# Kernel optimization log

Hardware: AMD Instinct MI355X
Metric: run time of the kernel (lower is better)

## Reference

```python
import jax, jax.numpy as jnp
import numpy as np

B, C, H, W = 8, 1, 384, 384
P, D, NH, L, E, HF = 16, 768, 12, 12, 4, 3072
Hp, Wp = H // P, W // P
N = Hp * Wp            # 576 tokens
DH = D // NH           # 64 per head
EPS = 1e-5


def setup_inputs() -> dict:
    key = jax.random.key(0)
    ks = jax.random.split(key, 10)
    g = lambda k, shp: (0.02 * jax.random.normal(k, shp, dtype=jnp.float32))
    return {
        "x": jax.random.normal(ks[0], (B, C, H, W), dtype=jnp.float32),
        "patch_w": g(ks[1], (D, C * P * P)),        # Conv2d(k=16,s=16) == unfold+matmul
        "patch_b": jnp.zeros((D,), jnp.float32),
        "pos_embed": g(ks[2], (1, N, D)),
        "ln1_g": jnp.ones((L, D), jnp.float32),
        "ln1_b": jnp.zeros((L, D), jnp.float32),
        "qkv_w": g(ks[3], (L, 3 * D, D)),           # torch MHA in_proj_weight
        "qkv_b": jnp.zeros((L, 3 * D), jnp.float32),
        "out_w": g(ks[4], (L, D, D)),
        "out_b": jnp.zeros((L, D), jnp.float32),
        "ln2_g": jnp.ones((L, D), jnp.float32),
        "ln2_b": jnp.zeros((L, D), jnp.float32),
        "gate_w": g(ks[5], (L, E, D)),
        "gate_b": jnp.zeros((L, E), jnp.float32),
        "w1": g(ks[6], (L, E, HF, D)),
        "b1": jnp.zeros((L, E, HF), jnp.float32),
        "w2": g(ks[7], (L, E, D, HF)),
        "b2": jnp.zeros((L, E, D), jnp.float32),
    }


def _ln(x, g, b):
    m = jnp.mean(x, -1, keepdims=True)
    v = jnp.var(x, -1, keepdims=True)
    return (x - m) * jax.lax.rsqrt(v + EPS) * g + b


def _layer(t, prm):
    (l1g, l1b, qw, qb, ow, ob, l2g, l2b, gw, gb, W1, B1, W2, B2) = prm
    # --- MHA (pre-LN, residual) ---
    h = _ln(t, l1g, l1b)
    qkv = h @ qw.T + qb                                   # [B,N,3D]
    q, k, v = jnp.split(qkv, 3, axis=-1)
    q = q.reshape(B, N, NH, DH).transpose(0, 2, 1, 3)     # [B,NH,N,DH]
    k = k.reshape(B, N, NH, DH).transpose(0, 2, 1, 3)
    v = v.reshape(B, N, NH, DH).transpose(0, 2, 1, 3)
    att = jax.nn.softmax(jnp.einsum('bhnd,bhmd->bhnm', q, k) / jnp.sqrt(jnp.float32(DH)), axis=-1)
    a = jnp.einsum('bhnm,bhmd->bhnd', att, v).transpose(0, 2, 1, 3).reshape(B, N, D)
    t = t + a @ ow.T + ob
    # --- MoE FFN, top_k=1: raw gate logits used as combine weights ---
    h2 = _ln(t, l2g, l2b)
    scores = h2 @ gw.T + gb                               # [B,N,E]
    idx = jnp.argmax(scores, axis=-1)                     # [B,N] chosen expert
    wgt = jnp.max(scores, axis=-1)                        # [B,N] raw logit weight
    hid = jax.nn.gelu(jnp.einsum('bnd,ehd->benh', h2, W1) + B1[None, :, None, :], approximate=False)
    y = jnp.einsum('benh,edh->bend', hid, W2) + B2[None, :, None, :]   # [B,E,N,D]
    sel = jax.nn.one_hot(idx, E, dtype=t.dtype) * wgt[..., None]       # [B,N,E]
    t = t + jnp.einsum('bend,bne->bnd', y, sel)
    return t, None


def reference(x, patch_w, patch_b, pos_embed, ln1_g, ln1_b, qkv_w, qkv_b,
              out_w, out_b, ln2_g, ln2_b, gate_w, gate_b, w1, b1, w2, b2):
    # patch embed: Conv2d(kernel=stride=P) == non-overlapping unfold + matmul
    patches = x.reshape(B, C, Hp, P, Wp, P).transpose(0, 2, 4, 1, 3, 5).reshape(B, N, C * P * P)
    tok = patches @ patch_w.T + patch_b + pos_embed
    layer = jax.checkpoint(_layer)
    tok, _ = jax.lax.scan(layer, tok,
                          (ln1_g, ln1_b, qkv_w, qkv_b, out_w, out_b,
                           ln2_g, ln2_b, gate_w, gate_b, w1, b1, w2, b2))
    # rearrange 'b (h w) c -> b c h w'
    return tok.reshape(B, Hp, Wp, D).transpose(0, 3, 1, 2)
```

## Files before the change

kernel.cpp:

```cpp
#include <hip/hip_runtime.h>
#include <cmath>

#define TOK 4608
#define DMODEL 768

typedef __attribute__((ext_vector_type(8))) _Float16 f16x8;
typedef __attribute__((ext_vector_type(4))) float f32x4;

__device__ __forceinline__ float gelu_exact(float x) {
    return 0.5f * x * (1.0f + erff(x * 0.70710678118654752440f));
}

__device__ __forceinline__ void cvt2(float x, unsigned short& h, unsigned short& m)
{
    _Float16 hf = (_Float16)x;
    float r = (x - (float)hf) * 2048.0f;
    _Float16 mf = (_Float16)r;
    h = __builtin_bit_cast(unsigned short, hf);
    m = __builtin_bit_cast(unsigned short, mf);
}

__device__ __forceinline__ void cvt2_pack8(const float4 a, const float4 b,
                                           uint4& H, uint4& M)
{
    unsigned short h[8], m[8];
    cvt2(a.x, h[0], m[0]); cvt2(a.y, h[1], m[1]);
    cvt2(a.z, h[2], m[2]); cvt2(a.w, h[3], m[3]);
    cvt2(b.x, h[4], m[4]); cvt2(b.y, h[5], m[5]);
    cvt2(b.z, h[6], m[6]); cvt2(b.w, h[7], m[7]);
    H = (uint4){ (unsigned)h[0] | ((unsigned)h[1] << 16), (unsigned)h[2] | ((unsigned)h[3] << 16),
                 (unsigned)h[4] | ((unsigned)h[5] << 16), (unsigned)h[6] | ((unsigned)h[7] << 16) };
    M = (uint4){ (unsigned)m[0] | ((unsigned)m[1] << 16), (unsigned)m[2] | ((unsigned)m[3] << 16),
                 (unsigned)m[4] | ((unsigned)m[5] << 16), (unsigned)m[6] | ((unsigned)m[7] << 16) };
}

__global__ __launch_bounds__(256)
void im2col_kernel(const float* __restrict__ x, float* __restrict__ patches)
{
    int idx = blockIdx.x*256 + threadIdx.x;
    int k = idx & 255, tokid = idx >> 8;
    int b = tokid / 576, n = tokid % 576;
    int hp = n / 24, wp = n % 24;
    patches[idx] = x[(size_t)b*147456 + (size_t)(hp*16 + (k >> 4))*384 + wp*16 + (k & 15)];
}

__global__ __launch_bounds__(256)
void ln_kernel(const float* __restrict__ in, float* __restrict__ out,
               const float* __restrict__ g, const float* __restrict__ bta)
{
    int tokid = blockIdx.x;
    const float* xr = in + (size_t)tokid*768;
    int t = threadIdx.x;
    float v0 = xr[t], v1 = xr[t+256], v2 = xr[t+512];
    float s = v0+v1+v2, q = v0*v0+v1*v1+v2*v2;
    for (int off = 32; off > 0; off >>= 1) {
        s += __shfl_down(s, off);
        q += __shfl_down(q, off);
    }
    __shared__ float ss[4], sq[4];
    int wv = t >> 6, ln = t & 63;
    if (ln == 0) { ss[wv] = s; sq[wv] = q; }
    __syncthreads();
    float ts = ss[0]+ss[1]+ss[2]+ss[3];
    float tq = sq[0]+sq[1]+sq[2]+sq[3];
    float mean = ts * (1.f/768.f);
    float var  = tq * (1.f/768.f) - mean*mean;
    float inv  = rsqrtf(var + 1e-5f);
    float* orow = out + (size_t)tokid*768;
    orow[t]     = (v0-mean)*inv*g[t]     + bta[t];
    orow[t+256] = (v1-mean)*inv*g[t+256] + bta[t+256];
    orow[t+512] = (v2-mean)*inv*g[t+512] + bta[t+512];
}

__global__ __launch_bounds__(256, 2)
void gemm_mfma(const float* __restrict__ A, const float* __restrict__ Bw,
               const float* __restrict__ bias, float* __restrict__ C,
               int M, int Nout, int K, int ldA, int ldC, int mode,
               const int* __restrict__ lists, const int* __restrict__ counts,
               const float* __restrict__ wgt)
{
    int Meff = M;
    const int* gather = nullptr;
    if (counts) {
        int e = blockIdx.z;
        Meff   = counts[e];
        gather = lists + e * TOK;
        Bw    += (size_t)e * Nout * K;
        bias  += (size_t)e * Nout;
    }
    int m0 = blockIdx.y << 7, n0 = blockIdx.x << 7;
    if (m0 >= Meff) return;

    __shared__ unsigned short Ah[128][40];
    __shared__ unsigned short Am[128][40];
    __shared__ unsigned short Bh[128][40];
    __shared__ unsigned short Bm[128][40];

    int t = threadIdx.x;
    int srow = t >> 1;
    int koff = (t & 1) << 4;

    int ar = m0 + srow;
    long agrow = -1;
    if (ar < Meff) agrow = gather ? gather[ar] : ar;
    const float* Asrc = (agrow >= 0) ? (A + (size_t)agrow*ldA + koff) : nullptr;
    const float* Bsrc = Bw + (size_t)(n0 + srow)*K + koff;

    int lane = t & 63;
    int wv   = t >> 6;
    int wm   = (wv >> 1) << 6;
    int wn   = (wv & 1) << 6;
    int r16  = lane & 15;
    int g    = lane >> 4;

    f32x4 acc1[4][4], acc2[4][4];
    #pragma unroll
    for (int i = 0; i < 4; ++i)
        #pragma unroll
        for (int j = 0; j < 4; ++j) {
            acc1[i][j] = (f32x4){0.f, 0.f, 0.f, 0.f};
            acc2[i][j] = (f32x4){0.f, 0.f, 0.f, 0.f};
        }

    float4 ra[4], rb[4];
    ra[0] = ra[1] = ra[2] = ra[3] = make_float4(0.f, 0.f, 0.f, 0.f);

    auto load_tile = [&](int k0) {
        if (Asrc) {
            ra[0] = *(const float4*)(Asrc + k0);
            ra[1] = *(const float4*)(Asrc + k0 + 4);
            ra[2] = *(const float4*)(Asrc + k0 + 8);
            ra[3] = *(const float4*)(Asrc + k0 + 12);
        }
        rb[0] = *(const float4*)(Bsrc + k0);
        rb[1] = *(const float4*)(Bsrc + k0 + 4);
        rb[2] = *(const float4*)(Bsrc + k0 + 8);
        rb[3] = *(const float4*)(Bsrc + k0 + 12);
    };

    auto stage = [&]() {
        uint4 H, M_;
        cvt2_pack8(ra[0], ra[1], H, M_);
        *(uint4*)&Ah[srow][koff]     = H;
        *(uint4*)&Am[srow][koff]     = M_;
        cvt2_pack8(ra[2], ra[3], H, M_);
        *(uint4*)&Ah[srow][koff + 8] = H;
        *(uint4*)&Am[srow][koff + 8] = M_;
        cvt2_pack8(rb[0], rb[1], H, M_);
        *(uint4*)&Bh[srow][koff]     = H;
        *(uint4*)&Bm[srow][koff]     = M_;
        cvt2_pack8(rb[2], rb[3], H, M_);
        *(uint4*)&Bh[srow][koff + 8] = H;
        *(uint4*)&Bm[srow][koff + 8] = M_;
    };

    load_tile(0);

    for (int k0 = 0; k0 < K; k0 += 32) {
        __syncthreads();
        stage();
        __syncthreads();
        if (k0 + 32 < K) load_tile(k0 + 32);

        f16x8 fah[4], fam[4];
        #pragma unroll
        for (int i = 0; i < 4; ++i) {
            int ml = wm + i*16 + r16;
            fah[i] = *(const f16x8*)&Ah[ml][g*8];
            fam[i] = *(const f16x8*)&Am[ml][g*8];
        }
        #pragma unroll
        for (int j = 0; j < 4; ++j) {
            int nl = wn + j*16 + r16;
            f16x8 fbh = *(const f16x8*)&Bh[nl][g*8];
            f16x8 fbm = *(const f16x8*)&Bm[nl][g*8];
            #pragma unroll
            for (int i = 0; i < 4; ++i) {
                acc1[i][j] = __builtin_amdgcn_mfma_f32_16x16x32_f16(fah[i], fbh, acc1[i][j], 0, 0, 0);
                acc2[i][j] = __builtin_amdgcn_mfma_f32_16x16x32_f16(fah[i], fbm, acc2[i][j], 0, 0, 0);
                acc2[i][j] = __builtin_amdgcn_mfma_f32_16x16x32_f16(fam[i], fbh, acc2[i][j], 0, 0, 0);
            }
        }
    }

    const float MS = 1.0f / 2048.0f;
    float biasv[4];
    #pragma unroll
    for (int j = 0; j < 4; ++j) biasv[j] = bias[n0 + wn + j*16 + r16];

    #pragma unroll
    for (int i = 0; i < 4; ++i) {
        int mb = m0 + wm + i*16 + (g << 2);
        #pragma unroll
        for (int r = 0; r < 4; ++r) {
            int m = mb + r;
            if (m >= Meff) continue;
            int row = gather ? gather[m] : m;
            float* crow = C + (size_t)row*ldC + n0 + wn + r16;
            float w = (mode == 3) ? wgt[row] : 0.f;
            #pragma unroll
            for (int j = 0; j < 4; ++j) {
                float val = acc1[i][j][r] + acc2[i][j][r] * MS + biasv[j];
                float* cp = crow + j*16;
                if      (mode == 0) *cp = val;
                else if (mode == 1) *cp += val;
                else if (mode == 2) *cp = gelu_exact(val);
                else if (mode == 3) *cp += w * val;
                else {
                    *cp = val + wgt[(size_t)(row % 576)*768 + n0 + wn + j*16 + r16];
                }
            }
        }
    }
}

__global__ __launch_bounds__(256)
void attn_kernel(const float* __restrict__ qkv, float* __restrict__ attn)
{
    int q0 = blockIdx.x << 6;
    int h  = blockIdx.y;
    int b  = blockIdx.z;
    const float* base = qkv + (size_t)b * 576 * 2304;
    int qoff = h << 6, koff = 768 + (h << 6), voff = 1536 + (h << 6);

    __shared__ unsigned short Qh[64][72], Qm[64][72];
    __shared__ unsigned short Kh[64][72], Km[64][72];
    __shared__ unsigned short Vth[64][72], Vtm[64][72];
    __shared__ unsigned short Ph[64][72], Pm[64][72];

    int t    = threadIdx.x;
    int lane = t & 63;
    int wq   = t >> 6;
    int l15  = lane & 15;
    int g    = lane >> 4;

    int srow = t >> 2;
    int sq   = t & 3;

    {
        const float* src = &base[(size_t)(q0 + srow)*2304 + qoff + (sq << 4)];
        #pragma unroll
        for (int k = 0; k < 16; k += 4) {
            float4 v = *(const float4*)(src + k);
            ushort4 hh, mm;
            cvt2(v.x, hh.x, mm.x); cvt2(v.y, hh.y, mm.y);
            cvt2(v.z, hh.z, mm.z); cvt2(v.w, hh.w, mm.w);
            *(ushort4*)&Qh[srow][(sq << 4) + k] = hh;
            *(ushort4*)&Qm[srow][(sq << 4) + k] = mm;
        }
    }
    __syncthreads();

    f16x8 fqh[2], fqm[2];
    #pragma unroll
    for (int ks = 0; ks < 2; ++ks) {
        fqh[ks] = *(const f16x8*)&Qh[wq*16 + l15][ks*32 + g*8];
        fqm[ks] = *(const f16x8*)&Qm[wq*16 + l15][ks*32 + g*8];
    }

    float4 rk[4], rv[4];
    {
        const float* ks_ = &base[(size_t)srow*2304 + koff + (sq << 4)];
        const float* vs_ = &base[(size_t)srow*2304 + voff + (sq << 2)];
        #pragma unroll
        for (int k = 0; k < 4; ++k) rk[k] = *(const float4*)(ks_ + 4*k);
        #pragma unroll
        for (int k = 0; k < 4; ++k) rv[k] = *(const float4*)(vs_ + 16*k);
    }

    f32x4 o1[4], o2[4];
    #pragma unroll
    for (int df = 0; df < 4; ++df) {
        o1[df] = (f32x4){0.f,0.f,0.f,0.f};
        o2[df] = (f32x4){0.f,0.f,0.f,0.f};
    }
    float m_[4] = {-3.4e38f,-3.4e38f,-3.4e38f,-3.4e38f};
    float l_[4] = {0.f,0.f,0.f,0.f};
    const float MS = 1.0f / 2048.0f;

    for (int j0 = 0; j0 < 576; j0 += 64) {
        __syncthreads();
        #pragma unroll
        for (int k = 0; k < 4; ++k) {
            ushort4 hh, mm;
            cvt2(rk[k].x, hh.x, mm.x); cvt2(rk[k].y, hh.y, mm.y);
            cvt2(rk[k].z, hh.z, mm.z); cvt2(rk[k].w, hh.w, mm.w);
            *(ushort4*)&Kh[srow][(sq << 4) + 4*k] = hh;
            *(ushort4*)&Km[srow][(sq << 4) + 4*k] = mm;
        }
        #pragma unroll
        for (int k = 0; k < 4; ++k) {
            ushort4 hh, mm;
            cvt2(rv[k].x, hh.x, mm.x); cvt2(rv[k].y, hh.y, mm.y);
            cvt2(rv[k].z, hh.z, mm.z); cvt2(rv[k].w, hh.w, mm.w);
            int dbase = (sq << 2) + (k << 4);
            Vth[dbase+0][srow] = hh.x; Vtm[dbase+0][srow] = mm.x;
            Vth[dbase+1][srow] = hh.y; Vtm[dbase+1][srow] = mm.y;
            Vth[dbase+2][srow] = hh.z; Vtm[dbase+2][srow] = mm.z;
            Vth[dbase+3][srow] = hh.w; Vtm[dbase+3][srow] = mm.w;
        }
        __syncthreads();
        int jn = j0 + 64;
        if (jn < 576) {
            const float* ks_ = &base[(size_t)(jn + srow)*2304 + koff + (sq << 4)];
            const float* vs_ = &base[(size_t)(jn + srow)*2304 + voff + (sq << 2)];
            #pragma unroll
            for (int k = 0; k < 4; ++k) rk[k] = *(const float4*)(ks_ + 4*k);
            #pragma unroll
            for (int k = 0; k < 4; ++k) rv[k] = *(const float4*)(vs_ + 16*k);
        }

        f32x4 s1[4], s2[4];
        #pragma unroll
        for (int jf = 0; jf < 4; ++jf) {
            s1[jf] = (f32x4){0.f,0.f,0.f,0.f};
            s2[jf] = (f32x4){0.f,0.f,0.f,0.f};
        }
        #pragma unroll
        for (int jf = 0; jf < 4; ++jf) {
            #pragma unroll
            for (int ks = 0; ks < 2; ++ks) {
                f16x8 fkh = *(const f16x8*)&Kh[jf*16 + l15][ks*32 + g*8];
                f16x8 fkm = *(const f16x8*)&Km[jf*16 + l15][ks*32 + g*8];
                s1[jf] = __builtin_amdgcn_mfma_f32_16x16x32_f16(fqh[ks], fkh, s1[jf], 0, 0, 0);
                s2[jf] = __builtin_amdgcn_mfma_f32_16x16x32_f16(fqh[ks], fkm, s2[jf], 0, 0, 0);
                s2[jf] = __builtin_amdgcn_mfma_f32_16x16x32_f16(fqm[ks], fkh, s2[jf], 0, 0, 0);
            }
        }
        float p[4][4];
        #pragma unroll
        for (int jf = 0; jf < 4; ++jf)
            #pragma unroll
            for (int r = 0; r < 4; ++r)
                p[jf][r] = (s1[jf][r] + s2[jf][r]*MS) * 0.125f;

        #pragma unroll
        for (int r = 0; r < 4; ++r) {
            float tm = fmaxf(fmaxf(p[0][r], p[1][r]), fmaxf(p[2][r], p[3][r]));
            #pragma unroll
            for (int off = 8; off > 0; off >>= 1) tm = fmaxf(tm, __shfl_xor(tm, off, 16));
            float mn = fmaxf(m_[r], tm);
            float f  = expf(m_[r] - mn);
            m_[r] = mn;
            l_[r] *= f;
            #pragma unroll
            for (int df = 0; df < 4; ++df) { o1[df][r] *= f; o2[df][r] *= f; }
            float ps = 0.f;
            #pragma unroll
            for (int jf = 0; jf < 4; ++jf) {
                p[jf][r] = expf(p[jf][r] - mn);
                ps += p[jf][r];
            }
            #pragma unroll
            for (int off = 8; off > 0; off >>= 1) ps += __shfl_xor(ps, off, 16);
            l_[r] += ps;
        }
        #pragma unroll
        for (int jf = 0; jf < 4; ++jf)
            #pragma unroll
            for (int r = 0; r < 4; ++r) {
                unsigned short ph, pm;
                cvt2(p[jf][r], ph, pm);
                Ph[wq*16 + g*4 + r][jf*16 + l15] = ph;
                Pm[wq*16 + g*4 + r][jf*16 + l15] = pm;
            }

        #pragma unroll
        for (int ks = 0; ks < 2; ++ks) {
            f16x8 fph = *(const f16x8*)&Ph[wq*16 + l15][ks*32 + g*8];
            f16x8 fpm = *(const f16x8*)&Pm[wq*16 + l15][ks*32 + g*8];
            #pragma unroll
            for (int df = 0; df < 4; ++df) {
                f16x8 fvh = *(const f16x8*)&Vth[df*16 + l15][ks*32 + g*8];
                f16x8 fvm = *(const f16x8*)&Vtm[df*16 + l15][ks*32 + g*8];
                o1[df] = __builtin_amdgcn_mfma_f32_16x16x32_f16(fph, fvh, o1[df], 0, 0, 0);
                o2[df] = __builtin_amdgcn_mfma_f32_16x16x32_f16(fph, fvm, o2[df], 0, 0, 0);
                o2[df] = __builtin_amdgcn_mfma_f32_16x16x32_f16(fpm, fvh, o2[df], 0, 0, 0);
            }
        }
    }

    #pragma unroll
    for (int r = 0; r < 4; ++r) {
        float inv = 1.f / l_[r];
        size_t row = (size_t)(b*576 + q0 + wq*16 + g*4 + r)*768 + qoff + l15;
        #pragma unroll
        for (int df = 0; df < 4; ++df)
            attn[row + df*16] = (o1[df][r] + o2[df][r]*MS) * inv;
    }
}

__global__ __launch_bounds__(256)
void gate_kernel(const float* __restrict__ h2, const float* __restrict__ gw,
                 const float* __restrict__ gb, float* __restrict__ wgt,
                 int* __restrict__ lists, int* __restrict__ counts)
{
    int tokid = blockIdx.x;
    int t = threadIdx.x;
    const float* hr = h2 + (size_t)tokid*768;
    float p0=0.f,p1=0.f,p2=0.f,p3=0.f;
    for (int k = t; k < 768; k += 256) {
        float hv = hr[k];
        p0 = fmaf(hv, gw[k],        p0);
        p1 = fmaf(hv, gw[768 + k],  p1);
        p2 = fmaf(hv, gw[1536 + k], p2);
        p3 = fmaf(hv, gw[2304 + k], p3);
    }
    for (int off = 32; off > 0; off >>= 1) {
        p0 += __shfl_down(p0, off);
        p1 += __shfl_down(p1, off);
        p2 += __shfl_down(p2, off);
        p3 += __shfl_down(p3, off);
    }
    __shared__ float red[4][4];
    int wv = t >> 6, ln = t & 63;
    if (ln == 0) { red[wv][0]=p0; red[wv][1]=p1; red[wv][2]=p2; red[wv][3]=p3; }
    __syncthreads();
    if (t == 0) {
        float s[4];
        #pragma unroll
        for (int e = 0; e < 4; ++e)
            s[e] = red[0][e]+red[1][e]+red[2][e]+red[3][e] + gb[e];
        int best = 0; float bv = s[0];
        #pragma unroll
        for (int e = 1; e < 4; ++e) if (s[e] > bv) { bv = s[e]; best = e; }
        wgt[tokid] = bv;
        int pos = atomicAdd(&counts[best], 1);
        lists[best*TOK + pos] = tokid;
    }
}

__global__ void zero_counts(int* counts) { if (threadIdx.x < 4) counts[threadIdx.x] = 0; }

__global__ __launch_bounds__(256)
void out_transpose(const float* __restrict__ tok, float* __restrict__ out)
{
    int idx = blockIdx.x*256 + threadIdx.x;
    int wp = idx % 24;
    int hp = (idx / 24) % 24;
    int d  = (idx / 576) % 768;
    int b  = idx / (576*768);
    out[idx] = tok[(size_t)(b*576 + hp*24 + wp)*768 + d];
}

extern "C" void kernel_launch(void* const* d_in, const int* in_sizes, int n_in,
                              void* d_out, int out_size, void* d_ws, size_t ws_size,
                              hipStream_t stream)
{
    const float* x       = (const float*)d_in[0];
    const float* patch_w = (const float*)d_in[1];
    const float* patch_b = (const float*)d_in[2];
    const float* pos     = (const float*)d_in[3];
    const float* ln1_g   = (const float*)d_in[4];
    const float* ln1_b   = (const float*)d_in[5];
    const float* qkv_w   = (const float*)d_in[6];
    const float* qkv_b   = (const float*)d_in[7];
    const float* out_w   = (const float*)d_in[8];
    const float* out_b   = (const float*)d_in[9];
    const float* ln2_g   = (const float*)d_in[10];
    const float* ln2_b   = (const float*)d_in[11];
    const float* gate_w  = (const float*)d_in[12];
    const float* gate_b  = (const float*)d_in[13];
    const float* w1      = (const float*)d_in[14];
    const float* b1      = (const float*)d_in[15];
    const float* w2      = (const float*)d_in[16];
    const float* b2      = (const float*)d_in[17];
    float* out = (float*)d_out;

    float* ws    = (float*)d_ws;
    float* tok   = ws;
    float* h     = ws + 3538944;
    float* scr   = ws + 7077888;
    float* qkv   = scr;
    float* attn  = scr + 10616832;
    float* hid   = scr;
    float* patches = scr;
    float* wgt   = ws + 21233664;
    int*   lists = (int*)(ws + 21238272);
    int*   counts= (int*)(ws + 21256704);

    im2col_kernel<<<4608, 256, 0, stream>>>(x, patches);
    gemm_mfma<<<dim3(6,36,1), 256, 0, stream>>>(patches, patch_w, patch_b, tok,
                                                4608, 768, 256, 256, 768, 4,
                                                nullptr, nullptr, pos);

    for (int l = 0; l < 12; ++l) {
        ln_kernel<<<4608, 256, 0, stream>>>(tok, h, ln1_g + l*768, ln1_b + l*768);
        gemm_mfma<<<dim3(18,36,1), 256, 0, stream>>>(h, qkv_w + (size_t)l*2304*768, qkv_b + l*2304,
                                                     qkv, 4608, 2304, 768, 768, 2304, 0,
                                                     nullptr, nullptr, nullptr);
        attn_kernel<<<dim3(9,12,8), 256, 0, stream>>>(qkv, attn);
        gemm_mfma<<<dim3(6,36,1), 256, 0, stream>>>(attn, out_w + (size_t)l*768*768, out_b + l*768,
                                                    tok, 4608, 768, 768, 768, 768, 1,
                                                    nullptr, nullptr, nullptr);
        ln_kernel<<<4608, 256, 0, stream>>>(tok, h, ln2_g + l*768, ln2_b + l*768);
        zero_counts<<<1, 64, 0, stream>>>(counts);
        gate_kernel<<<4608, 256, 0, stream>>>(h, gate_w + l*3072, gate_b + l*4, wgt, lists, counts);
        gemm_mfma<<<dim3(24,36,4), 256, 0, stream>>>(h, w1 + (size_t)l*4*3072*768, b1 + (size_t)l*4*3072,
                                                     hid, 4608, 3072, 768, 768, 3072, 2,
                                                     lists, counts, nullptr);
        gemm_mfma<<<dim3(6,36,4), 256, 0, stream>>>(hid, w2 + (size_t)l*4*768*3072, b2 + (size_t)l*4*768,
                                                    tok, 4608, 768, 3072, 3072, 768, 3,
                                                    lists, counts, wgt);
    }
    out_transpose<<<13824, 256, 0, stream>>>(tok, out);
}
```

Before: 8.237 ms.

## Store activations and weights as pre-split fp16 hi/lo planes for GEMM and attention

Each producer kernel (LN, QKV GEMM, attention, W1 GEMM with GELU, im2col) now writes its output as two fp16 planes (high part and scaled residual) instead of fp32. Weights are converted into the same two-plane form once per layer by a new cvt_plane kernel. The GEMM and attention inner loops then copy these planes straight into shared memory with no per-tile conversion, and the activation traffic they read is about halved. In exchange there are extra conversion launches and a weight pass every layer (w1/w2 are large), plus more workspace.

```diff
diff --git a/kernel.cpp b/kernel.cpp
--- a/kernel.cpp
+++ b/kernel.cpp
@@ -6,6 +6,7 @@
 
 typedef __attribute__((ext_vector_type(8))) _Float16 f16x8;
 typedef __attribute__((ext_vector_type(4))) float f32x4;
+typedef unsigned short ushort_t;
 
 __device__ __forceinline__ float gelu_exact(float x) {
     return 0.5f * x * (1.0f + erff(x * 0.70710678118654752440f));
@@ -20,32 +21,41 @@
     m = __builtin_bit_cast(unsigned short, mf);
 }
 
-__device__ __forceinline__ void cvt2_pack8(const float4 a, const float4 b,
-                                           uint4& H, uint4& M)
-{
-    unsigned short h[8], m[8];
-    cvt2(a.x, h[0], m[0]); cvt2(a.y, h[1], m[1]);
-    cvt2(a.z, h[2], m[2]); cvt2(a.w, h[3], m[3]);
-    cvt2(b.x, h[4], m[4]); cvt2(b.y, h[5], m[5]);
-    cvt2(b.z, h[6], m[6]); cvt2(b.w, h[7], m[7]);
-    H = (uint4){ (unsigned)h[0] | ((unsigned)h[1] << 16), (unsigned)h[2] | ((unsigned)h[3] << 16),
-                 (unsigned)h[4] | ((unsigned)h[5] << 16), (unsigned)h[6] | ((unsigned)h[7] << 16) };
-    M = (uint4){ (unsigned)m[0] | ((unsigned)m[1] << 16), (unsigned)m[2] | ((unsigned)m[3] << 16),
-                 (unsigned)m[4] | ((unsigned)m[5] << 16), (unsigned)m[6] | ((unsigned)m[7] << 16) };
+__device__ __forceinline__ float tof(unsigned short u) {
+    return (float)__builtin_bit_cast(_Float16, u);
 }
 
 __global__ __launch_bounds__(256)
-void im2col_kernel(const float* __restrict__ x, float* __restrict__ patches)
+void cvt_plane(const float* __restrict__ src, ushort_t* __restrict__ dh,
+               ushort_t* __restrict__ dm, int n)
+{
+    int i = (blockIdx.x*256 + threadIdx.x) << 2;
+    if (i >= n) return;
+    float4 v = *(const float4*)(src + i);
+    ushort4 H, M;
+    cvt2(v.x, H.x, M.x); cvt2(v.y, H.y, M.y);
+    cvt2(v.z, H.z, M.z); cvt2(v.w, H.w, M.w);
+    *(ushort4*)(dh + i) = H;
+    *(ushort4*)(dm + i) = M;
+}
+
+__global__ __launch_bounds__(256)
+void im2col_kernel(const float* __restrict__ x, ushort_t* __restrict__ ph,
+                   ushort_t* __restrict__ pm)
 {
     int idx = blockIdx.x*256 + threadIdx.x;
     int k = idx & 255, tokid = idx >> 8;
     int b = tokid / 576, n = tokid % 576;
     int hp = n / 24, wp = n % 24;
-    patches[idx] = x[(size_t)b*147456 + (size_t)(hp*16 + (k >> 4))*384 + wp*16 + (k & 15)];
+    float v = x[(size_t)b*147456 + (size_t)(hp*16 + (k >> 4))*384 + wp*16 + (k & 15)];
+    unsigned short hh, mm;
+    cvt2(v, hh, mm);
+    ph[idx] = hh; pm[idx] = mm;
 }
 
 __global__ __launch_bounds__(256)
-void ln_kernel(const float* __restrict__ in, float* __restrict__ out,
+void ln_kernel(const float* __restrict__ in, ushort_t* __restrict__ outh,
+               ushort_t* __restrict__ outm,
                const float* __restrict__ g, const float* __restrict__ bta)
 {
     int tokid = blockIdx.x;
@@ -66,15 +76,21 @@
     float mean = ts * (1.f/768.f);
     float var  = tq * (1.f/768.f) - mean*mean;
     float inv  = rsqrtf(var + 1e-5f);
-    float* orow = out + (size_t)tokid*768;
-    orow[t]     = (v0-mean)*inv*g[t]     + bta[t];
-    orow[t+256] = (v1-mean)*inv*g[t+256] + bta[t+256];
-    orow[t+512] = (v2-mean)*inv*g[t+512] + bta[t+512];
+    size_t base = (size_t)tokid*768;
+    unsigned short hh, mm;
+    float y0 = (v0-mean)*inv*g[t]     + bta[t];
+    float y1 = (v1-mean)*inv*g[t+256] + bta[t+256];
+    float y2 = (v2-mean)*inv*g[t+512] + bta[t+512];
+    cvt2(y0, hh, mm); outh[base+t]     = hh; outm[base+t]     = mm;
+    cvt2(y1, hh, mm); outh[base+t+256] = hh; outm[base+t+256] = mm;
+    cvt2(y2, hh, mm); outh[base+t+512] = hh; outm[base+t+512] = mm;
 }
 
 __global__ __launch_bounds__(256, 2)
-void gemm_mfma(const float* __restrict__ A, const float* __restrict__ Bw,
+void gemm_mfma(const ushort_t* __restrict__ Ahp, const ushort_t* __restrict__ Amp,
+               const ushort_t* __restrict__ Bhp, const ushort_t* __restrict__ Bmp,
                const float* __restrict__ bias, float* __restrict__ C,
+               ushort_t* __restrict__ Chp, ushort_t* __restrict__ Cmp,
                int M, int Nout, int K, int ldA, int ldC, int mode,
                const int* __restrict__ lists, const int* __restrict__ counts,
                const float* __restrict__ wgt)
@@ -85,7 +101,8 @@
         int e = blockIdx.z;
         Meff   = counts[e];
         gather = lists + e * TOK;
-        Bw    += (size_t)e * Nout * K;
+        Bhp   += (size_t)e * Nout * K;
+        Bmp   += (size_t)e * Nout * K;
         bias  += (size_t)e * Nout;
     }
     int m0 = blockIdx.y << 7, n0 = blockIdx.x << 7;
@@ -103,8 +120,10 @@
     int ar = m0 + srow;
     long agrow = -1;
     if (ar < Meff) agrow = gather ? gather[ar] : ar;
-    const float* Asrc = (agrow >= 0) ? (A + (size_t)agrow*ldA + koff) : nullptr;
-    const float* Bsrc = Bw + (size_t)(n0 + srow)*K + koff;
+    const ushort_t* Ah_src = (agrow >= 0) ? (Ahp + (size_t)agrow*ldA + koff) : nullptr;
+    const ushort_t* Am_src = (agrow >= 0) ? (Amp + (size_t)agrow*ldA + koff) : nullptr;
+    const ushort_t* Bh_src = Bhp + (size_t)(n0 + srow)*K + koff;
+    const ushort_t* Bm_src = Bmp + (size_t)(n0 + srow)*K + koff;
 
     int lane = t & 63;
     int wv   = t >> 6;
@@ -122,43 +141,34 @@
             acc2[i][j] = (f32x4){0.f, 0.f, 0.f, 0.f};
         }
 
-    float4 ra[4], rb[4];
-    ra[0] = ra[1] = ra[2] = ra[3] = make_float4(0.f, 0.f, 0.f, 0.f);
+    uint4 rah[2], ram[2], rbh[2], rbm[2];
+    rah[0] = rah[1] = ram[0] = ram[1] = (uint4){0u,0u,0u,0u};
 
     auto load_tile = [&](int k0) {
-        if (Asrc) {
-            ra[0] = *(const float4*)(Asrc + k0);
-            ra[1] = *(const float4*)(Asrc + k0 + 4);
-            ra[2] = *(const float4*)(Asrc + k0 + 8);
-            ra[3] = *(const float4*)(Asrc + k0 + 12);
-        }
-        rb[0] = *(const float4*)(Bsrc + k0);
-        rb[1] = *(const float4*)(Bsrc + k0 + 4);
-        rb[2] = *(const float4*)(Bsrc + k0 + 8);
-        rb[3] = *(const float4*)(Bsrc + k0 + 12);
-    };
-
-    auto stage = [&]() {
-        uint4 H, M_;
-        cvt2_pack8(ra[0], ra[1], H, M_);
-        *(uint4*)&Ah[srow][koff]     = H;
-        *(uint4*)&Am[srow][koff]     = M_;
-        cvt2_pack8(ra[2], ra[3], H, M_);
-        *(uint4*)&Ah[srow][koff + 8] = H;
-        *(uint4*)&Am[srow][koff + 8] = M_;
-        cvt2_pack8(rb[0], rb[1], H, M_);
-        *(uint4*)&Bh[srow][koff]     = H;
-        *(uint4*)&Bm[srow][koff]     = M_;
-        cvt2_pack8(rb[2], rb[3], H, M_);
-        *(uint4*)&Bh[srow][koff + 8] = H;
-        *(uint4*)&Bm[srow][koff + 8] = M_;
+        if (Ah_src) {
+            rah[0] = *(const uint4*)(Ah_src + k0);
+            rah[1] = *(const uint4*)(Ah_src + k0 + 8);
+            ram[0] = *(const uint4*)(Am_src + k0);
+            ram[1] = *(const uint4*)(Am_src + k0 + 8);
+        }
+        rbh[0] = *(const uint4*)(Bh_src + k0);
+        rbh[1] = *(const uint4*)(Bh_src + k0 + 8);
+        rbm[0] = *(const uint4*)(Bm_src + k0);
+        rbm[1] = *(const uint4*)(Bm_src + k0 + 8);
     };
 
     load_tile(0);
 
     for (int k0 = 0; k0 < K; k0 += 32) {
         __syncthreads();
-        stage();
+        *(uint4*)&Ah[srow][koff]   = rah[0];
+        *(uint4*)&Ah[srow][koff+8] = rah[1];
+        *(uint4*)&Am[srow][koff]   = ram[0];
+        *(uint4*)&Am[srow][koff+8] = ram[1];
+        *(uint4*)&Bh[srow][koff]   = rbh[0];
+        *(uint4*)&Bh[srow][koff+8] = rbh[1];
+        *(uint4*)&Bm[srow][koff]   = rbm[0];
+        *(uint4*)&Bm[srow][koff+8] = rbm[1];
         __syncthreads();
         if (k0 + 32 < K) load_tile(k0 + 32);
 
@@ -196,18 +206,26 @@
             int m = mb + r;
             if (m >= Meff) continue;
             int row = gather ? gather[m] : m;
-            float* crow = C + (size_t)row*ldC + n0 + wn + r16;
+            size_t rowoff = (size_t)row*ldC + n0 + wn + r16;
             float w = (mode == 3) ? wgt[row] : 0.f;
             #pragma unroll
             for (int j = 0; j < 4; ++j) {
                 float val = acc1[i][j][r] + acc2[i][j][r] * MS + biasv[j];
-                float* cp = crow + j*16;
-                if      (mode == 0) *cp = val;
-                else if (mode == 1) *cp += val;
-                else if (mode == 2) *cp = gelu_exact(val);
-                else if (mode == 3) *cp += w * val;
-                else {
-                    *cp = val + wgt[(size_t)(row % 576)*768 + n0 + wn + j*16 + r16];
+                size_t off = rowoff + j*16;
+                if (mode == 0) {
+                    unsigned short hh, mm;
+                    cvt2(val, hh, mm);
+                    Chp[off] = hh; Cmp[off] = mm;
+                } else if (mode == 1) {
+                    C[off] += val;
+                } else if (mode == 2) {
+                    unsigned short hh, mm;
+                    cvt2(gelu_exact(val), hh, mm);
+                    Chp[off] = hh; Cmp[off] = mm;
+                } else if (mode == 3) {
+                    C[off] += w * val;
+                } else {
+                    C[off] = val + wgt[(size_t)(row % 576)*768 + n0 + wn + j*16 + r16];
                 }
             }
         }
@@ -215,13 +233,14 @@
 }
 
 __global__ __launch_bounds__(256)
-void attn_kernel(const float* __restrict__ qkv, float* __restrict__ attn)
+void attn_kernel(const ushort_t* __restrict__ qh, const ushort_t* __restrict__ qm,
+                 ushort_t* __restrict__ aoh, ushort_t* __restrict__ aom)
 {
     int q0 = blockIdx.x << 6;
     int h  = blockIdx.y;
     int b  = blockIdx.z;
-    const float* base = qkv + (size_t)b * 576 * 2304;
-    int qoff = h << 6, koff = 768 + (h << 6), voff = 1536 + (h << 6);
+    size_t bbase = (size_t)b * 576 * 2304;
+    int qoff = h << 6, koff2 = 768 + (h << 6), voff = 1536 + (h << 6);
 
     __shared__ unsigned short Qh[64][72], Qm[64][72];
     __shared__ unsigned short Kh[64][72], Km[64][72];
@@ -238,16 +257,12 @@
     int sq   = t & 3;
 
     {
-        const float* src = &base[(size_t)(q0 + srow)*2304 + qoff + (sq << 4)];
-        #pragma unroll
-        for (int k = 0; k < 16; k += 4) {
-            float4 v = *(const float4*)(src + k);
-            ushort4 hh, mm;
-            cvt2(v.x, hh.x, mm.x); cvt2(v.y, hh.y, mm.y);
-            cvt2(v.z, hh.z, mm.z); cvt2(v.w, hh.w, mm.w);
-            *(ushort4*)&Qh[srow][(sq << 4) + k] = hh;
-            *(ushort4*)&Qm[srow][(sq << 4) + k] = mm;
-        }
+        const ushort_t* sh = qh + bbase + (size_t)(q0 + srow)*2304 + qoff + (sq << 4);
+        const ushort_t* sm = qm + bbase + (size_t)(q0 + srow)*2304 + qoff + (sq << 4);
+        *(uint4*)&Qh[srow][(sq<<4)]   = *(const uint4*)(sh);
+        *(uint4*)&Qh[srow][(sq<<4)+8] = *(const uint4*)(sh + 8);
+        *(uint4*)&Qm[srow][(sq<<4)]   = *(const uint4*)(sm);
+        *(uint4*)&Qm[srow][(sq<<4)+8] = *(const uint4*)(sm + 8);
     }
     __syncthreads();
 
@@ -258,15 +273,22 @@
         fqm[ks] = *(const f16x8*)&Qm[wq*16 + l15][ks*32 + g*8];
     }
 
-    float4 rk[4], rv[4];
-    {
-        const float* ks_ = &base[(size_t)srow*2304 + koff + (sq << 4)];
-        const float* vs_ = &base[(size_t)srow*2304 + voff + (sq << 2)];
-        #pragma unroll
-        for (int k = 0; k < 4; ++k) rk[k] = *(const float4*)(ks_ + 4*k);
-        #pragma unroll
-        for (int k = 0; k < 4; ++k) rv[k] = *(const float4*)(vs_ + 16*k);
-    }
+    uint4 pkh[2], pkm[2];
+    uint2 pvh[4], pvm[4];
+    auto fetch_kv = [&](int j0) {
+        const ushort_t* kh_ = qh + bbase + (size_t)(j0 + srow)*2304 + koff2 + (sq << 4);
+        const ushort_t* km_ = qm + bbase + (size_t)(j0 + srow)*2304 + koff2 + (sq << 4);
+        pkh[0] = *(const uint4*)(kh_);     pkh[1] = *(const uint4*)(kh_ + 8);
+        pkm[0] = *(const uint4*)(km_);     pkm[1] = *(const uint4*)(km_ + 8);
+        const ushort_t* vh_ = qh + bbase + (size_t)(j0 + srow)*2304 + voff + (sq << 2);
+        const ushort_t* vm_ = qm + bbase + (size_t)(j0 + srow)*2304 + voff + (sq << 2);
+        #pragma unroll
+        for (int k = 0; k < 4; ++k) {
+            pvh[k] = *(const uint2*)(vh_ + (k << 4));
+            pvm[k] = *(const uint2*)(vm_ + (k << 4));
+        }
+    };
+    fetch_kv(0);
 
     f32x4 o1[4], o2[4];
     #pragma unroll
@@ -280,35 +302,23 @@
 
     for (int j0 = 0; j0 < 576; j0 += 64) {
         __syncthreads();
+        *(uint4*)&Kh[srow][(sq<<4)]   = pkh[0];
+        *(uint4*)&Kh[srow][(sq<<4)+8] = pkh[1];
+        *(uint4*)&Km[srow][(sq<<4)]   = pkm[0];
+        *(uint4*)&Km[srow][(sq<<4)+8] = pkm[1];
         #pragma unroll
         for (int k = 0; k < 4; ++k) {
-            ushort4 hh, mm;
-            cvt2(rk[k].x, hh.x, mm.x); cvt2(rk[k].y, hh.y, mm.y);
-            cvt2(rk[k].z, hh.z, mm.z); cvt2(rk[k].w, hh.w, mm.w);
-            *(ushort4*)&Kh[srow][(sq << 4) + 4*k] = hh;
-            *(ushort4*)&Km[srow][(sq << 4) + 4*k] = mm;
-        }
-        #pragma unroll
-        for (int k = 0; k < 4; ++k) {
-            ushort4 hh, mm;
-            cvt2(rv[k].x, hh.x, mm.x); cvt2(rv[k].y, hh.y, mm.y);
-            cvt2(rv[k].z, hh.z, mm.z); cvt2(rv[k].w, hh.w, mm.w);
+            const ushort_t* ph = (const ushort_t*)&pvh[k];
+            const ushort_t* pm = (const ushort_t*)&pvm[k];
             int dbase = (sq << 2) + (k << 4);
-            Vth[dbase+0][srow] = hh.x; Vtm[dbase+0][srow] = mm.x;
-            Vth[dbase+1][srow] = hh.y; Vtm[dbase+1][srow] = mm.y;
-            Vth[dbase+2][srow] = hh.z; Vtm[dbase+2][srow] = mm.z;
-            Vth[dbase+3][srow] = hh.w; Vtm[dbase+3][srow] = mm.w;
+            Vth[dbase+0][srow] = ph[0]; Vtm[dbase+0][srow] = pm[0];
+            Vth[dbase+1][srow] = ph[1]; Vtm[dbase+1][srow] = pm[1];
+            Vth[dbase+2][srow] = ph[2]; Vtm[dbase+2][srow] = pm[2];
+            Vth[dbase+3][srow] = ph[3]; Vtm[dbase+3][srow] = pm[3];
         }
         __syncthreads();
         int jn = j0 + 64;
-        if (jn < 576) {
-            const float* ks_ = &base[(size_t)(jn + srow)*2304 + koff + (sq << 4)];
-            const float* vs_ = &base[(size_t)(jn + srow)*2304 + voff + (sq << 2)];
-            #pragma unroll
-            for (int k = 0; k < 4; ++k) rk[k] = *(const float4*)(ks_ + 4*k);
-            #pragma unroll
-            for (int k = 0; k < 4; ++k) rv[k] = *(const float4*)(vs_ + 16*k);
-        }
+        if (jn < 576) fetch_kv(jn);
 
         f32x4 s1[4], s2[4];
         #pragma unroll
@@ -383,24 +393,31 @@
     #pragma unroll
     for (int r = 0; r < 4; ++r) {
         float inv = 1.f / l_[r];
-        size_t row = (size_t)(b*576 + q0 + wq*16 + g*4 + r)*768 + qoff + l15;
-        #pragma unroll
-        for (int df = 0; df < 4; ++df)
-            attn[row + df*16] = (o1[df][r] + o2[df][r]*MS) * inv;
+        size_t rowoff = (size_t)(b*576 + q0 + wq*16 + g*4 + r)*768 + qoff + l15;
+        #pragma unroll
+        for (int df = 0; df < 4; ++df) {
+            float ov = (o1[df][r] + o2[df][r]*MS) * inv;
+            unsigned short hh, mm;
+            cvt2(ov, hh, mm);
+            aoh[rowoff + df*16] = hh;
+            aom[rowoff + df*16] = mm;
+        }
     }
 }
 
 __global__ __launch_bounds__(256)
-void gate_kernel(const float* __restrict__ h2, const float* __restrict__ gw,
-                 const float* __restrict__ gb, float* __restrict__ wgt,
-                 int* __restrict__ lists, int* __restrict__ counts)
+void gate_kernel(const ushort_t* __restrict__ hh, const ushort_t* __restrict__ hm,
+                 const float* __restrict__ gw, const float* __restrict__ gb,
+                 float* __restrict__ wgt, int* __restrict__ lists, int* __restrict__ counts)
 {
     int tokid = blockIdx.x;
     int t = threadIdx.x;
-    const float* hr = h2 + (size_t)tokid*768;
+    const ushort_t* hrh = hh + (size_t)tokid*768;
+    const ushort_t* hrm = hm + (size_t)tokid*768;
+    const float MS = 1.0f / 2048.0f;
     float p0=0.f,p1=0.f,p2=0.f,p3=0.f;
     for (int k = t; k < 768; k += 256) {
-        float hv = hr[k];
+        float hv = tof(hrh[k]) + tof(hrm[k]) * MS;
         p0 = fmaf(hv, gw[k],        p0);
         p1 = fmaf(hv, gw[768 + k],  p1);
         p2 = fmaf(hv, gw[1536 + k], p2);
@@ -467,40 +484,62 @@
     const float* b2      = (const float*)d_in[17];
     float* out = (float*)d_out;
 
-    float* ws    = (float*)d_ws;
-    float* tok   = ws;
-    float* h     = ws + 3538944;
-    float* scr   = ws + 7077888;
-    float* qkv   = scr;
-    float* attn  = scr + 10616832;
-    float* hid   = scr;
-    float* patches = scr;
-    float* wgt   = ws + 21233664;
-    int*   lists = (int*)(ws + 21238272);
-    int*   counts= (int*)(ws + 21256704);
-
-    im2col_kernel<<<4608, 256, 0, stream>>>(x, patches);
-    gemm_mfma<<<dim3(6,36,1), 256, 0, stream>>>(patches, patch_w, patch_b, tok,
+    char* wsb = (char*)d_ws;
+    size_t OF = 0;
+    float*    tok   = (float*)(wsb + OF);    OF += 14155776;
+    ushort_t* h_h   = (ushort_t*)(wsb + OF); OF += 7077888;
+    ushort_t* h_m   = (ushort_t*)(wsb + OF); OF += 7077888;
+    ushort_t* qkvh  = (ushort_t*)(wsb + OF); OF += 21233664;
+    ushort_t* qkvm  = (ushort_t*)(wsb + OF); OF += 21233664;
+    ushort_t* at_h  = (ushort_t*)(wsb + OF); OF += 7077888;
+    ushort_t* at_m  = (ushort_t*)(wsb + OF); OF += 7077888;
+    ushort_t* hid_h = (ushort_t*)(wsb + OF); OF += 28311552;
+    ushort_t* hid_m = (ushort_t*)(wsb + OF); OF += 28311552;
+    ushort_t* w_h   = (ushort_t*)(wsb + OF); OF += 42467328;
+    ushort_t* w_m   = (ushort_t*)(wsb + OF); OF += 42467328;
+    float*    wgt   = (float*)(wsb + OF);    OF += 18432;
+    int*      lists = (int*)(wsb + OF);      OF += 73728;
+    int*      counts= (int*)(wsb + OF);      OF += 16;
+
+    const size_t SEG_QKV = 0;
+    const size_t SEG_OUT = 1769472;
+    const size_t SEG_W1  = SEG_OUT + 589824;
+    const size_t SEG_W2  = SEG_W1  + 9437184;
+
+    im2col_kernel<<<4608, 256, 0, stream>>>(x, hid_h, hid_m);
+    cvt_plane<<<192, 256, 0, stream>>>(patch_w, w_h, w_m, 196608);
+    gemm_mfma<<<dim3(6,36,1), 256, 0, stream>>>(hid_h, hid_m, w_h, w_m, patch_b,
+                                                tok, nullptr, nullptr,
                                                 4608, 768, 256, 256, 768, 4,
                                                 nullptr, nullptr, pos);
 
     for (int l = 0; l < 12; ++l) {
-        ln_kernel<<<4608, 256, 0, stream>>>(tok, h, ln1_g + l*768, ln1_b + l*768);
-        gemm_mfma<<<dim3(18,36,1), 256, 0, stream>>>(h, qkv_w + (size_t)l*2304*768, qkv_b + l*2304,
-                                                     qkv, 4608, 2304, 768, 768, 2304, 0,
+        cvt_plane<<<1728, 256, 0, stream>>>(qkv_w + (size_t)l*1769472, w_h + SEG_QKV, w_m + SEG_QKV, 1769472);
+        cvt_plane<<< 576, 256, 0, stream>>>(out_w + (size_t)l*589824,  w_h + SEG_OUT, w_m + SEG_OUT, 589824);
+        cvt_plane<<<9216, 256, 0, stream>>>(w1 + (size_t)l*9437184,    w_h + SEG_W1,  w_m + SEG_W1,  9437184);
+        cvt_plane<<<9216, 256, 0, stream>>>(w2 + (size_t)l*9437184,    w_h + SEG_W2,  w_m + SEG_W2,  9437184);
+
+        ln_kernel<<<4608, 256, 0, stream>>>(tok, h_h, h_m, ln1_g + l*768, ln1_b + l*768);
+        gemm_mfma<<<dim3(18,36,1), 256, 0, stream>>>(h_h, h_m, w_h + SEG_QKV, w_m + SEG_QKV,
+                                                     qkv_b + l*2304, nullptr, qkvh, qkvm,
+                                                     4608, 2304, 768, 768, 2304, 0,
                                                      nullptr, nullptr, nullptr);
-        attn_kernel<<<dim3(9,12,8), 256, 0, stream>>>(qkv, attn);
-        gemm_mfma<<<dim3(6,36,1), 256, 0, stream>>>(attn, out_w + (size_t)l*768*768, out_b + l*768,
-                                                    tok, 4608, 768, 768, 768, 768, 1,
+        attn_kernel<<<dim3(9,12,8), 256, 0, stream>>>(qkvh, qkvm, at_h, at_m);
+        gemm_mfma<<<dim3(6,36,1), 256, 0, stream>>>(at_h, at_m, w_h + SEG_OUT, w_m + SEG_OUT,
+                                                    out_b + l*768, tok, nullptr, nullptr,
+                                                    4608, 768, 768, 768, 768, 1,
                                                     nullptr, nullptr, nullptr);
-        ln_kernel<<<4608, 256, 0, stream>>>(tok, h, ln2_g + l*768, ln2_b + l*768);
+        ln_kernel<<<4608, 256, 0, stream>>>(tok, h_h, h_m, ln2_g + l*768, ln2_b + l*768);
         zero_counts<<<1, 64, 0, stream>>>(counts);
-        gate_kernel<<<4608, 256, 0, stream>>>(h, gate_w + l*3072, gate_b + l*4, wgt, lists, counts);
-        gemm_mfma<<<dim3(24,36,4), 256, 0, stream>>>(h, w1 + (size_t)l*4*3072*768, b1 + (size_t)l*4*3072,
-                                                     hid, 4608, 3072, 768, 768, 3072, 2,
+        gate_kernel<<<4608, 256, 0, stream>>>(h_h, h_m, gate_w + l*3072, gate_b + l*4,
+                                              wgt, lists, counts);
+        gemm_mfma<<<dim3(24,36,4), 256, 0, stream>>>(h_h, h_m, w_h + SEG_W1, w_m + SEG_W1,
+                                                     b1 + (size_t)l*4*3072, nullptr, hid_h, hid_m,
+                                                     4608, 3072, 768, 768, 3072, 2,
                                                      lists, counts, nullptr);
-        gemm_mfma<<<dim3(6,36,4), 256, 0, stream>>>(hid, w2 + (size_t)l*4*768*3072, b2 + (size_t)l*4*768,
-                                                    tok, 4608, 768, 3072, 3072, 768, 3,
+        gemm_mfma<<<dim3(6,36,4), 256, 0, stream>>>(hid_h, hid_m, w_h + SEG_W2, w_m + SEG_W2,
+                                                    b2 + (size_t)l*4*768, tok, nullptr, nullptr,
+                                                    4608, 768, 3072, 3072, 768, 3,
                                                     lists, counts, wgt);
     }
     out_transpose<<<13824, 256, 0, stream>>>(tok, out);
```

Result: slower. 11.87 ms (+44.1%).

## Split GEMM into 128-tile and 64-tile variants with workgroup swizzle

Applied to the files above, without the earlier changes.

Replaces the single 128x128 GEMM with two templated kernels. gemm_big keeps 128x128 tiles for the QKV and W1 projections. gemm_small uses 64x64 tiles with a 64-deep K step for the N=768 GEMMs (patch embed, out-proj, W2), which gives those launches more workgroups and better CU fill. An optional block-ID swizzle remaps workgroup order across 8 groups, likely targeting the MI355X's XCD dispatch so neighbouring tiles share cache. Occupancy hint is raised to 3. The small tiles trade more global reloads of A and B for the extra parallelism.

```diff
diff --git a/kernel.cpp b/kernel.cpp
--- a/kernel.cpp
+++ b/kernel.cpp
@@ -72,12 +72,13 @@
     orow[t+512] = (v2-mean)*inv*g[t+512] + bta[t+512];
 }
 
-__global__ __launch_bounds__(256, 2)
-void gemm_mfma(const float* __restrict__ A, const float* __restrict__ Bw,
-               const float* __restrict__ bias, float* __restrict__ C,
-               int M, int Nout, int K, int ldA, int ldC, int mode,
-               const int* __restrict__ lists, const int* __restrict__ counts,
-               const float* __restrict__ wgt)
+template<bool SWZ>
+__global__ __launch_bounds__(256, 3)
+void gemm_big(const float* __restrict__ A, const float* __restrict__ Bw,
+              const float* __restrict__ bias, float* __restrict__ C,
+              int M, int Nout, int K, int ldA, int ldC, int mode,
+              const int* __restrict__ lists, const int* __restrict__ counts,
+              const float* __restrict__ wgt)
 {
     int Meff = M;
     const int* gather = nullptr;
@@ -88,7 +89,13 @@
         Bw    += (size_t)e * Nout * K;
         bias  += (size_t)e * Nout;
     }
-    int m0 = blockIdx.y << 7, n0 = blockIdx.x << 7;
+    int gx  = gridDim.x;
+    int bid = blockIdx.y * gx + blockIdx.x;
+    if constexpr (SWZ) {
+        int nwg = gx * gridDim.y;
+        bid = (bid & 7) * (nwg >> 3) + (bid >> 3);
+    }
+    int m0 = (bid / gx) << 7, n0 = (bid % gx) << 7;
     if (m0 >= Meff) return;
 
     __shared__ unsigned short Ah[128][40];
@@ -138,27 +145,25 @@
         rb[3] = *(const float4*)(Bsrc + k0 + 12);
     };
 
-    auto stage = [&]() {
-        uint4 H, M_;
-        cvt2_pack8(ra[0], ra[1], H, M_);
-        *(uint4*)&Ah[srow][koff]     = H;
-        *(uint4*)&Am[srow][koff]     = M_;
-        cvt2_pack8(ra[2], ra[3], H, M_);
-        *(uint4*)&Ah[srow][koff + 8] = H;
-        *(uint4*)&Am[srow][koff + 8] = M_;
-        cvt2_pack8(rb[0], rb[1], H, M_);
-        *(uint4*)&Bh[srow][koff]     = H;
-        *(uint4*)&Bm[srow][koff]     = M_;
-        cvt2_pack8(rb[2], rb[3], H, M_);
-        *(uint4*)&Bh[srow][koff + 8] = H;
-        *(uint4*)&Bm[srow][koff + 8] = M_;
-    };
-
     load_tile(0);
 
     for (int k0 = 0; k0 < K; k0 += 32) {
         __syncthreads();
-        stage();
+        {
+            uint4 H, M_;
+            cvt2_pack8(ra[0], ra[1], H, M_);
+            *(uint4*)&Ah[srow][koff]   = H;
+            *(uint4*)&Am[srow][koff]   = M_;
+            cvt2_pack8(ra[2], ra[3], H, M_);
+            *(uint4*)&Ah[srow][koff+8] = H;
+            *(uint4*)&Am[srow][koff+8] = M_;
+            cvt2_pack8(rb[0], rb[1], H, M_);
+            *(uint4*)&Bh[srow][koff]   = H;
+            *(uint4*)&Bm[srow][koff]   = M_;
+            cvt2_pack8(rb[2], rb[3], H, M_);
+            *(uint4*)&Bh[srow][koff+8] = H;
+            *(uint4*)&Bm[srow][koff+8] = M_;
+        }
         __syncthreads();
         if (k0 + 32 < K) load_tile(k0 + 32);
 
@@ -196,19 +201,165 @@
             int m = mb + r;
             if (m >= Meff) continue;
             int row = gather ? gather[m] : m;
-            float* crow = C + (size_t)row*ldC + n0 + wn + r16;
+            size_t rowoff = (size_t)row*ldC + n0 + wn + r16;
             float w = (mode == 3) ? wgt[row] : 0.f;
             #pragma unroll
             for (int j = 0; j < 4; ++j) {
                 float val = acc1[i][j][r] + acc2[i][j][r] * MS + biasv[j];
-                float* cp = crow + j*16;
-                if      (mode == 0) *cp = val;
-                else if (mode == 1) *cp += val;
-                else if (mode == 2) *cp = gelu_exact(val);
-                else if (mode == 3) *cp += w * val;
-                else {
-                    *cp = val + wgt[(size_t)(row % 576)*768 + n0 + wn + j*16 + r16];
+                size_t off = rowoff + j*16;
+                if      (mode == 0) C[off] = val;
+                else if (mode == 1) C[off] += val;
+                else if (mode == 2) C[off] = gelu_exact(val);
+                else if (mode == 3) C[off] += w * val;
+                else C[off] = val + wgt[(size_t)(row % 576)*768 + n0 + wn + j*16 + r16];
+            }
+        }
+    }
+}
+
+template<bool SWZ>
+__global__ __launch_bounds__(256, 3)
+void gemm_small(const float* __restrict__ A, const float* __restrict__ Bw,
+                const float* __restrict__ bias, float* __restrict__ C,
+                int M, int Nout, int K, int ldA, int ldC, int mode,
+                const int* __restrict__ lists, const int* __restrict__ counts,
+                const float* __restrict__ wgt)
+{
+    int Meff = M;
+    const int* gather = nullptr;
+    if (counts) {
+        int e = blockIdx.z;
+        Meff   = counts[e];
+        gather = lists + e * TOK;
+        Bw    += (size_t)e * Nout * K;
+        bias  += (size_t)e * Nout;
+    }
+    int gx  = gridDim.x;
+    int bid = blockIdx.y * gx + blockIdx.x;
+    if constexpr (SWZ) {
+        int nwg = gx * gridDim.y;
+        bid = (bid & 7) * (nwg >> 3) + (bid >> 3);
+    }
+    int m0 = (bid / gx) << 6, n0 = (bid % gx) << 6;
+    if (m0 >= Meff) return;
+
+    __shared__ unsigned short Ah[64][72];
+    __shared__ unsigned short Am[64][72];
+    __shared__ unsigned short Bh[64][72];
+    __shared__ unsigned short Bm[64][72];
+
+    int t = threadIdx.x;
+    int srow  = t >> 1;
+    int khalf = (t & 1) << 5;
+    bool isA = srow < 64;
+    int row  = isA ? srow : (srow - 64);
+
+    const float* src = nullptr;
+    if (isA) {
+        int ar = m0 + row;
+        if (ar < Meff) {
+            long agrow = gather ? gather[ar] : ar;
+            src = A + (size_t)agrow*ldA + khalf;
+        }
+    } else {
+        src = Bw + (size_t)(n0 + row)*K + khalf;
+    }
+
+    int lane = t & 63;
+    int wv   = t >> 6;
+    int wm   = (wv >> 1) << 5;
+    int wn   = (wv & 1) << 5;
+    int r16  = lane & 15;
+    int g    = lane >> 4;
+
+    f32x4 acc1[2][2], acc2[2][2];
+    #pragma unroll
+    for (int i = 0; i < 2; ++i)
+        #pragma unroll
+        for (int j = 0; j < 2; ++j) {
+            acc1[i][j] = (f32x4){0.f, 0.f, 0.f, 0.f};
+            acc2[i][j] = (f32x4){0.f, 0.f, 0.f, 0.f};
+        }
+
+    float4 rr[8];
+    #pragma unroll
+    for (int i = 0; i < 8; ++i) rr[i] = make_float4(0.f, 0.f, 0.f, 0.f);
+
+    auto load_tile = [&](int k0) {
+        if (src) {
+            #pragma unroll
+            for (int i = 0; i < 8; ++i) rr[i] = *(const float4*)(src + k0 + 4*i);
+        }
+    };
+
+    load_tile(0);
+
+    for (int k0 = 0; k0 < K; k0 += 64) {
+        __syncthreads();
+        {
+            unsigned short (*Xh)[72] = isA ? Ah : Bh;
+            unsigned short (*Xm)[72] = isA ? Am : Bm;
+            #pragma unroll
+            for (int i = 0; i < 8; i += 2) {
+                uint4 H, M_;
+                cvt2_pack8(rr[i], rr[i+1], H, M_);
+                *(uint4*)&Xh[row][khalf + 4*i] = H;
+                *(uint4*)&Xm[row][khalf + 4*i] = M_;
+            }
+        }
+        __syncthreads();
+        if (k0 + 64 < K) load_tile(k0 + 64);
+
+        #pragma unroll
+        for (int ks = 0; ks < 2; ++ks) {
+            f16x8 fah[2], fam[2];
+            #pragma unroll
+            for (int i = 0; i < 2; ++i) {
+                int ml = wm + i*16 + r16;
+                fah[i] = *(const f16x8*)&Ah[ml][ks*32 + g*8];
+                fam[i] = *(const f16x8*)&Am[ml][ks*32 + g*8];
+            }
+            #pragma unroll
+            for (int j = 0; j < 2; ++j) {
+                int nl = wn + j*16 + r16;
+                f16x8 fbh = *(const f16x8*)&Bh[nl][ks*32 + g*8];
+                f16x8 fbm = *(const f16x8*)&Bm[nl][ks*32 + g*8];
+                #pragma unroll
+                for (int i = 0; i < 2; ++i) {
+                    acc1[i][j] = __builtin_amdgcn_mfma_f32_16x16x32_f16(fah[i], fbh, acc1[i][j], 0, 0, 0);
+                    acc2[i][j] = __builtin_amdgcn_mfma_f32_16x16x32_f16(fah[i], fbm, acc2[i][j], 0, 0, 0);
+                    acc2[i][j] = __builtin_amdgcn_mfma_f32_16x16x32_f16(fam[i], fbh, acc2[i][j], 0, 0, 0);
                 }
+            }
+        }
+    }
+
+    const float MS = 1.0f / 2048.0f;
+    float biasv[2];
+    #pragma unroll
+    for (int j = 0; j < 2; ++j) biasv[j] = bias[n0 + wn + j*16 + r16];
+
+    #pragma unroll
+    for (int i = 0; i < 2; ++i) {
+        int mb = m0 + wm + i*16 + (g << 2);
+        #pragma unroll
+        for (int r = 0; r < 2*2; ++r) { }
+        #pragma unroll
+        for (int r = 0; r < 4; ++r) {
+            int m = mb + r;
+            if (m >= Meff) continue;
+            int rowc = gather ? gather[m] : m;
+            size_t rowoff = (size_t)rowc*ldC + n0 + wn + r16;
+            float w = (mode == 3) ? wgt[rowc] : 0.f;
+            #pragma unroll
+            for (int j = 0; j < 2; ++j) {
+                float val = acc1[i][j][r] + acc2[i][j][r] * MS + biasv[j];
+                size_t off = rowoff + j*16;
+                if      (mode == 0) C[off] = val;
+                else if (mode == 1) C[off] += val;
+                else if (mode == 2) C[off] = gelu_exact(val);
+                else if (mode == 3) C[off] += w * val;
+                else C[off] = val + wgt[(size_t)(rowc % 576)*768 + n0 + wn + j*16 + r16];
             }
         }
     }
@@ -480,28 +631,32 @@
     int*   counts= (int*)(ws + 21256704);
 
     im2col_kernel<<<4608, 256, 0, stream>>>(x, patches);
-    gemm_mfma<<<dim3(6,36,1), 256, 0, stream>>>(patches, patch_w, patch_b, tok,
-                                                4608, 768, 256, 256, 768, 4,
-                                                nullptr, nullptr, pos);
+    gemm_small<true><<<dim3(12,72,1), 256, 0, stream>>>(patches, patch_w, patch_b, tok,
+                                                        4608, 768, 256, 256, 768, 4,
+                                                        nullptr, nullptr, pos);
 
     for (int l = 0; l < 12; ++l) {
         ln_kernel<<<4608, 256, 0, stream>>>(tok, h, ln1_g + l*768, ln1_b + l*768);
-        gemm_mfma<<<dim3(18,36,1), 256, 0, stream>>>(h, qkv_w + (size_t)l*2304*768, qkv_b + l*2304,
-                                                     qkv, 4608, 2304, 768, 768, 2304, 0,
-                                                     nullptr, nullptr, nullptr);
+        gemm_big<true><<<dim3(18,36,1), 256, 0, stream>>>(h, qkv_w + (size_t)l*2304*768,
+                                                          qkv_b + l*2304, qkv,
+                                                          4608, 2304, 768, 768, 2304, 0,
+                                                          nullptr, nullptr, nullptr);
         attn_kernel<<<dim3(9,12,8), 256, 0, stream>>>(qkv, attn);
-        gemm_mfma<<<dim3(6,36,1), 256, 0, stream>>>(attn, out_w + (size_t)l*768*768, out_b + l*768,
-                                                    tok, 4608, 768, 768, 768, 768, 1,
-                                                    nullptr, nullptr, nullptr);
+        gemm_small<true><<<dim3(12,72,1), 256, 0, stream>>>(attn, out_w + (size_t)l*589824,
+                                                            out_b + l*768, tok,
+                                                            4608, 768, 768, 768, 768, 1,
+                                                            nullptr, nullptr, nullptr);
         ln_kernel<<<4608, 256, 0, stream>>>(tok, h, ln2_g + l*768, ln2_b + l*768);
         zero_counts<<<1, 64, 0, stream>>>(counts);
         gate_kernel<<<4608, 256, 0, stream>>>(h, gate_w + l*3072, gate_b + l*4, wgt, lists, counts);
-        gemm_mfma<<<dim3(24,36,4), 256, 0, stream>>>(h, w1 + (size_t)l*4*3072*768, b1 + (size_t)l*4*3072,
-                                                     hid, 4608, 3072, 768, 768, 3072, 2,
-                                                     lists, counts, nullptr);
-        gemm_mfma<<<dim3(6,36,4), 256, 0, stream>>>(hid, w2 + (size_t)l*4*768*3072, b2 + (size_t)l*4*768,
-                                                    tok, 4608, 768, 3072, 3072, 768, 3,
-                                                    lists, counts, wgt);
+        gemm_big<false><<<dim3(24,36,4), 256, 0, stream>>>(h, w1 + (size_t)l*9437184,
+                                                           b1 + (size_t)l*4*3072, hid,
+                                                           4608, 3072, 768, 768, 3072, 2,
+                                                           lists, counts, nullptr);
+        gemm_small<false><<<dim3(12,72,4), 256, 0, stream>>>(hid, w2 + (size_t)l*9437184,
+                                                             b2 + (size_t)l*4*768, tok,
+                                                             4608, 768, 3072, 3072, 768, 3,
+                                                             lists, counts, wgt);
     }
     out_transpose<<<13824, 256, 0, stream>>>(tok, out);
 }
```

New measurement: 15.65 ms. +90.1%, slower.
